# Kernel optimization log

Hardware: AMD Instinct MI355X
Metric: run time of the kernel (lower is better)

## Reference

```python
import jax, jax.numpy as jnp
import numpy as np

L, D_IN, D_HID, D_OUT, N = 8, 256, 1024, 256, 32768


def setup_inputs() -> dict:
    key = jax.random.key(0)
    kx, kp, kw1, kw2 = jax.random.split(key, 4)
    x = jax.random.normal(kx, (N, D_IN), dtype=jnp.float32)
    plane_idx = jax.random.randint(kp, (N,), 0, L, dtype=jnp.int32)
    W1 = jax.random.normal(kw1, (L, D_HID, D_IN), dtype=jnp.float32) * 0.014
    b1 = jnp.zeros((L, D_HID), dtype=jnp.float32)
    W2 = jax.random.normal(kw2, (L, D_OUT, D_HID), dtype=jnp.float32) * np.float32((2.0 / D_HID) ** 0.5)
    b2 = jnp.zeros((L, D_OUT), dtype=jnp.float32)
    return {"x": x, "W1": W1, "b1": b1, "W2": W2, "b2": b2, "plane_idx": plane_idx}


def reference(x, W1, b1, W2, b2, plane_idx):
    # Dense-dispatch MoE reference: scan over the L planes, run the full
    # 2-layer MLP for each plane's weights, and select per-walker rows via
    # the plane mask (equivalent math to gather -> MLP -> scatter).
    n_planes = W1.shape[0]
    out0 = jnp.zeros((x.shape[0], W2.shape[1]), dtype=x.dtype)

    def plane_step(out, p):
        h = jax.nn.gelu(x @ W1[p].T + b1[p], approximate=False)  # [N, D_hid]
        o = h @ W2[p].T + b2[p]                                  # [N, D_out]
        out = jnp.where((plane_idx == p)[:, None], o, out)
        return out, None

    out, _ = jax.lax.scan(plane_step, out0, jnp.arange(n_planes))
    return out
```

## Files before the change

kernel.cpp:

```cpp
#include <hip/hip_runtime.h>
#include <hip/hip_fp16.h>
#include <cstdint>

#define NT      32768
#define DIN     256
#define DHID    1024
#define DOUT    256
#define NPLANES 8
#define NBLK    (NT / 256)

typedef unsigned short u16;
typedef __attribute__((ext_vector_type(8))) _Float16 f16x8;
typedef __attribute__((ext_vector_type(4))) float    f32x4;

#define WS_OFFSETS 0
#define WS_META    64
#define WS_TP      1024
#define WS_TM      (WS_TP + 544*4)
#define WS_BLKHIST (WS_TM + 544*4)
#define WS_BLKBASE (WS_BLKHIST + NBLK*8*4)
#define WS_PERM    (WS_BLKBASE + NBLK*8*4)
#define WS_XB      (WS_PERM + NT*4)
#define WS_W1B     (WS_XB + NT*DIN*2)
#define WS_W2B     (WS_W1B + NPLANES*DHID*DIN*2)
#define WS_HB      (WS_W2B + NPLANES*DOUT*DHID*2)

__device__ __forceinline__ u16 f2h_bits(float f) {
    __half h = __float2half(f);
    return *reinterpret_cast<u16*>(&h);
}

__device__ __forceinline__ void gl_lds16(const void* g, void* l) {
    __builtin_amdgcn_global_load_lds(
        (const __attribute__((address_space(1))) void*)g,
        (__attribute__((address_space(3))) void*)l,
        16, 0, 0);
}

__global__ void prep_k(const int* __restrict__ pidx, const float* __restrict__ x,
                       const float* __restrict__ W1, const float* __restrict__ W2,
                       int* __restrict__ blkhist, u16* __restrict__ xb,
                       u16* __restrict__ w1b, u16* __restrict__ w2b) {
    __shared__ int cnt[NPLANES];
    const int t = threadIdx.x, lane = t & 63;
    if ((int)blockIdx.x < NBLK) {
        if (t < NPLANES) cnt[t] = 0;
        __syncthreads();
        const int p = pidx[blockIdx.x * 256 + t];
#pragma unroll
        for (int q = 0; q < NPLANES; ++q) {
            unsigned long long m = __ballot(p == q);
            if (p == q && __popcll(m & ((1ULL << lane) - 1)) == 0)
                atomicAdd(&cnt[q], __popcll(m));
        }
        __syncthreads();
        if (t < NPLANES) blkhist[blockIdx.x * NPLANES + t] = cnt[t];
    }
    const int n0 = NT * DIN / 4, n1 = NPLANES * DHID * DIN / 4, n2 = NPLANES * DOUT * DHID / 4;
    const int stride = gridDim.x * blockDim.x;
    for (int i = blockIdx.x * blockDim.x + t; i < n0 + n1 + n2; i += stride) {
        const float4* s; ushort4* d; int j;
        if (i < n0)           { s = (const float4*)x;  d = (ushort4*)xb;  j = i; }
        else if (i < n0 + n1) { s = (const float4*)W1; d = (ushort4*)w1b; j = i - n0; }
        else                  { s = (const float4*)W2; d = (ushort4*)w2b; j = i - n0 - n1; }
        float4 v = s[j];
        ushort4 o;
        o.x = f2h_bits(v.x); o.y = f2h_bits(v.y);
        o.z = f2h_bits(v.z); o.w = f2h_bits(v.w);
        d[j] = o;
    }
}

__global__ void scan_k(const int* __restrict__ blkhist, int* __restrict__ offsets,
                       int* __restrict__ blkbase, int* __restrict__ meta,
                       int* __restrict__ tp, int* __restrict__ tm) {
    __shared__ int tot[NPLANES];
    const int t = threadIdx.x;
    if (t < NPLANES) {
        int s = 0;
#pragma unroll 8
        for (int b = 0; b < NBLK; ++b) s += blkhist[b * NPLANES + t];
        tot[t] = s;
    }
    __syncthreads();
    if (t == 0) {
        int off = 0, tc = 0;
        for (int p = 0; p < NPLANES; ++p) {
            offsets[p] = off;
            for (int m = 0; m < tot[p]; m += 64) { tp[tc] = p; tm[tc] = m; ++tc; }
            off += tot[p];
        }
        offsets[NPLANES] = off;
        meta[0] = tc;
    }
    __syncthreads();
    if (t < NPLANES) {
        int run = offsets[t];
#pragma unroll 8
        for (int b = 0; b < NBLK; ++b) {
            blkbase[b * NPLANES + t] = run;
            run += blkhist[b * NPLANES + t];
        }
    }
}

__global__ void scatter_k(const int* __restrict__ pidx, const int* __restrict__ blkbase,
                          int* __restrict__ perm) {
    __shared__ int wcnt[4][NPLANES];
    __shared__ int wbase[4][NPLANES];
    const int t = threadIdx.x, lane = t & 63, wave = t >> 6;
    const int i = blockIdx.x * 256 + t;
    const int p = pidx[i];
    int rank = 0;
#pragma unroll
    for (int q = 0; q < NPLANES; ++q) {
        unsigned long long m = __ballot(p == q);
        if (lane == 0) wcnt[wave][q] = __popcll(m);
        if (p == q) rank = __popcll(m & ((1ULL << lane) - 1));
    }
    __syncthreads();
    if (t < NPLANES) {
        int run = blkbase[blockIdx.x * NPLANES + t];
#pragma unroll
        for (int w = 0; w < 4; ++w) { wbase[w][t] = run; run += wcnt[w][t]; }
    }
    __syncthreads();
    perm[wbase[wave][p] + rank] = i;
}

#define XCD_MAP(NSPLIT)                                                        \
    const int ntiles = meta[0];                                                \
    const int xcd = blockIdx.x & 7, idx = blockIdx.x >> 3;                     \
    const int q8 = ntiles >> 3, r8 = ntiles & 7;                               \
    const int tn = q8 + (xcd < r8 ? 1 : 0);                                    \
    if (idx >= tn * (NSPLIT)) return;                                          \
    const int tile = (xcd < r8 ? xcd * (q8 + 1)                                \
                               : r8 * (q8 + 1) + (xcd - r8) * q8)              \
                     + idx / (NSPLIT);                                         \
    const int n0v = (idx % (NSPLIT)) * 128;

__global__ __launch_bounds__(256, 4) void gemm1_k(
    const u16* __restrict__ xb, const u16* __restrict__ w1b,
    const float* __restrict__ b1, const int* __restrict__ perm,
    const int* __restrict__ offsets, const int* __restrict__ meta,
    const int* __restrict__ tp, const int* __restrict__ tm,
    u16* __restrict__ hb)
{
    __shared__ __align__(16) u16 smem[12288];
    XCD_MAP(8)
    const int p   = tp[tile];
    const int m0  = tm[tile];
    const int off = offsets[p];
    const int cnt = offsets[p + 1] - off;

    u16* const sA = smem;
    u16* const sB = smem + 4096;

    const int tid = threadIdx.x;
    const u16* aptr[2];
    const u16* bptr[4];
#pragma unroll
    for (int c = 0; c < 2; ++c) {
        const int slot = c * 256 + tid, row = slot >> 3, ch = slot & 7;
        const int gr = min(m0 + row, cnt - 1);
        aptr[c] = xb + (size_t)perm[off + gr] * DIN + ((ch ^ (row & 7)) * 8);
    }
#pragma unroll
    for (int c = 0; c < 4; ++c) {
        const int slot = c * 256 + tid, row = slot >> 3, ch = slot & 7;
        bptr[c] = w1b + ((size_t)p * DHID + n0v + row) * DIN + ((ch ^ (row & 7)) * 8);
    }
    const int wave = tid >> 6, lane = tid & 63;
    const int wr = wave >> 1, wc = wave & 1;
    const int lm = lane & 15, lk = lane >> 4;

    f32x4 acc[2][4];
#pragma unroll
    for (int a = 0; a < 2; ++a)
#pragma unroll
        for (int b = 0; b < 4; ++b) acc[a][b] = (f32x4){0.f, 0.f, 0.f, 0.f};

    for (int kt = 0; kt < DIN / 64; ++kt) {
        const int k0 = kt * 64;
#pragma unroll
        for (int c = 0; c < 2; ++c) gl_lds16(aptr[c] + k0, sA + c * 2048 + tid * 8);
#pragma unroll
        for (int c = 0; c < 4; ++c) gl_lds16(bptr[c] + k0, sB + c * 2048 + tid * 8);
        __syncthreads();
#pragma unroll
        for (int kk = 0; kk < 2; ++kk) {
            f16x8 af[2], bf[4];
#pragma unroll
            for (int mf = 0; mf < 2; ++mf) {
                const int row = wr * 32 + mf * 16 + lm;
                const int g   = kk * 4 + lk;
                af[mf] = *(const f16x8*)(sA + row * 64 + ((g ^ (row & 7)) * 8));
            }
#pragma unroll
            for (int nf = 0; nf < 4; ++nf) {
                const int row = wc * 64 + nf * 16 + lm;
                const int g   = kk * 4 + lk;
                bf[nf] = *(const f16x8*)(sB + row * 64 + ((g ^ (row & 7)) * 8));
            }
#pragma unroll
            for (int mf = 0; mf < 2; ++mf)
#pragma unroll
                for (int nf = 0; nf < 4; ++nf)
                    acc[mf][nf] = __builtin_amdgcn_mfma_f32_16x16x32_f16(
                        af[mf], bf[nf], acc[mf][nf], 0, 0, 0);
        }
        __syncthreads();
    }

    u16* const sOut = smem;
#pragma unroll
    for (int nf = 0; nf < 4; ++nf) {
        const int col = wc * 64 + nf * 16 + lm;
        const float bb = b1[p * DHID + n0v + col];
        const int cc = col >> 3, c7 = col & 7;
#pragma unroll
        for (int mf = 0; mf < 2; ++mf) {
#pragma unroll
            for (int j = 0; j < 4; ++j) {
                const int tok = wr * 32 + mf * 16 + lk * 4 + j;
                float v = acc[mf][nf][j] + bb;
                float g = 0.5f * v * (1.0f + erff(v * 0.70710678118654752f));
                sOut[tok * 128 + ((cc ^ (tok & 15)) * 8) + c7] = f2h_bits(g);
            }
        }
    }
    __syncthreads();
    const int r = tid >> 2, qq = tid & 3;
    if (m0 + r < cnt) {
        u16* dst = hb + (size_t)(off + m0 + r) * DHID + n0v;
#pragma unroll
        for (int c = 0; c < 4; ++c) {
            const int l = qq * 4 + c;
            *(int4*)(dst + l * 8) = *(const int4*)(sOut + r * 128 + ((l ^ (r & 15)) * 8));
        }
    }
}

__global__ __launch_bounds__(256, 4) void gemm2_k(
    const u16* __restrict__ hb, const u16* __restrict__ w2b,
    const float* __restrict__ b2, const int* __restrict__ perm,
    const int* __restrict__ offsets, const int* __restrict__ meta,
    const int* __restrict__ tp, const int* __restrict__ tm,
    float* __restrict__ out)
{
    __shared__ __align__(16) u16 smem[12288];
    XCD_MAP(2)
    const int p   = tp[tile];
    const int m0  = tm[tile];
    const int off = offsets[p];
    const int cnt = offsets[p + 1] - off;

    u16* const sA = smem;
    u16* const sB = smem + 4096;

    const int tid = threadIdx.x;
    const u16* aptr[2];
    const u16* bptr[4];
#pragma unroll
    for (int c = 0; c < 2; ++c) {
        const int slot = c * 256 + tid, row = slot >> 3, ch = slot & 7;
        aptr[c] = hb + (size_t)(off + min(m0 + row, cnt - 1)) * DHID + ((ch ^ (row & 7)) * 8);
    }
#pragma unroll
    for (int c = 0; c < 4; ++c) {
        const int slot = c * 256 + tid, row = slot >> 3, ch = slot & 7;
        bptr[c] = w2b + ((size_t)p * DOUT + n0v + row) * DHID + ((ch ^ (row & 7)) * 8);
    }
    const int wave = tid >> 6, lane = tid & 63;
    const int wr = wave >> 1, wc = wave & 1;
    const int lm = lane & 15, lk = lane >> 4;

    f32x4 acc[2][4];
#pragma unroll
    for (int a = 0; a < 2; ++a)
#pragma unroll
        for (int b = 0; b < 4; ++b) acc[a][b] = (f32x4){0.f, 0.f, 0.f, 0.f};

    for (int kt = 0; kt < DHID / 64; ++kt) {
        const int k0 = kt * 64;
#pragma unroll
        for (int c = 0; c < 2; ++c) gl_lds16(aptr[c] + k0, sA + c * 2048 + tid * 8);
#pragma unroll
        for (int c = 0; c < 4; ++c) gl_lds16(bptr[c] + k0, sB + c * 2048 + tid * 8);
        __syncthreads();
#pragma unroll
        for (int kk = 0; kk < 2; ++kk) {
            f16x8 af[2], bf[4];
#pragma unroll
            for (int mf = 0; mf < 2; ++mf) {
                const int row = wr * 32 + mf * 16 + lm;
                const int g   = kk * 4 + lk;
                af[mf] = *(const f16x8*)(sA + row * 64 + ((g ^ (row & 7)) * 8));
            }
#pragma unroll
            for (int nf = 0; nf < 4; ++nf) {
                const int row = wc * 64 + nf * 16 + lm;
                const int g   = kk * 4 + lk;
                bf[nf] = *(const f16x8*)(sB + row * 64 + ((g ^ (row & 7)) * 8));
            }
#pragma unroll
            for (int mf = 0; mf < 2; ++mf)
#pragma unroll
                for (int nf = 0; nf < 4; ++nf)
                    acc[mf][nf] = __builtin_amdgcn_mfma_f32_16x16x32_f16(
                        af[mf], bf[nf], acc[mf][nf], 0, 0, 0);
        }
        __syncthreads();
    }

#pragma unroll
    for (int nf = 0; nf < 4; ++nf) {
        const int col = n0v + wc * 64 + nf * 16 + lm;
        const float bb = b2[p * DOUT + col];
#pragma unroll
        for (int mf = 0; mf < 2; ++mf) {
#pragma unroll
            for (int j = 0; j < 4; ++j) {
                const int tok = wr * 32 + mf * 16 + lk * 4 + j;
                if (m0 + tok < cnt)
                    out[(size_t)perm[off + m0 + tok] * DOUT + col] = acc[mf][nf][j] + bb;
            }
        }
    }
}

extern "C" void kernel_launch(void* const* d_in, const int* in_sizes, int n_in,
                              void* d_out, int out_size, void* d_ws, size_t ws_size,
                              hipStream_t stream) {
    const float* x    = (const float*)d_in[0];
    const float* W1   = (const float*)d_in[1];
    const float* b1   = (const float*)d_in[2];
    const float* W2   = (const float*)d_in[3];
    const float* b2   = (const float*)d_in[4];
    const int*   pidx = (const int*)d_in[5];
    float*       out  = (float*)d_out;

    char* ws      = (char*)d_ws;
    int* offsets  = (int*)(ws + WS_OFFSETS);
    int* meta     = (int*)(ws + WS_META);
    int* tp       = (int*)(ws + WS_TP);
    int* tm       = (int*)(ws + WS_TM);
    int* blkhist  = (int*)(ws + WS_BLKHIST);
    int* blkbase  = (int*)(ws + WS_BLKBASE);
    int* perm     = (int*)(ws + WS_PERM);
    u16* xb       = (u16*)(ws + WS_XB);
    u16* w1b      = (u16*)(ws + WS_W1B);
    u16* w2b      = (u16*)(ws + WS_W2B);
    u16* hb       = (u16*)(ws + WS_HB);

    prep_k<<<2048, 256, 0, stream>>>(pidx, x, W1, W2, blkhist, xb, w1b, w2b);
    scan_k<<<1, 64, 0, stream>>>(blkhist, offsets, blkbase, meta, tp, tm);
    scatter_k<<<NBLK, 256, 0, stream>>>(pidx, blkbase, perm);

    gemm1_k<<<4224, 256, 0, stream>>>(xb, w1b, b1, perm, offsets, meta, tp, tm, hb);
    gemm2_k<<<1056, 256, 0, stream>>>(hb, w2b, b2, perm, offsets, meta, tp, tm, out);
}
```

Measured before the change: 115.5 us.

## Double-buffer gemm2 LDS loads, use sigmoid GELU approximation, retune launch bounds

The second GEMM now stages tiles into two LDS buffers, issuing global-to-LDS loads for the next K step before computing the current one. Partial vmcnt waits with raw barriers replace the full __syncthreads, so load latency can overlap MFMA work. The exact erf GELU in gemm1's epilogue is replaced by a tanh-form approximation built from exp and a hardware reciprocal, which cuts epilogue cost but changes numerics slightly. Launch bounds change to 6 waves/SIMD occupancy hints for gemm1 and 3 for gemm2, since the doubled LDS footprint lowers gemm2 occupancy.

```diff
diff --git a/kernel.cpp b/kernel.cpp
--- a/kernel.cpp
+++ b/kernel.cpp
@@ -35,6 +35,12 @@
         (const __attribute__((address_space(1))) void*)g,
         (__attribute__((address_space(3))) void*)l,
         16, 0, 0);
+}
+
+__device__ __forceinline__ float gelu_fast(float x) {
+    const float u = x * (1.5957691216f + 0.07135481283f * x * x);
+    const float e = __expf(-u);
+    return x * __builtin_amdgcn_rcpf(1.0f + e);
 }
 
 __global__ void prep_k(const int* __restrict__ pidx, const float* __restrict__ x,
@@ -139,7 +145,7 @@
                      + idx / (NSPLIT);                                         \
     const int n0v = (idx % (NSPLIT)) * 128;
 
-__global__ __launch_bounds__(256, 4) void gemm1_k(
+__global__ __launch_bounds__(256, 6) void gemm1_k(
     const u16* __restrict__ xb, const u16* __restrict__ w1b,
     const float* __restrict__ b1, const int* __restrict__ perm,
     const int* __restrict__ offsets, const int* __restrict__ meta,
@@ -223,9 +229,8 @@
 #pragma unroll
             for (int j = 0; j < 4; ++j) {
                 const int tok = wr * 32 + mf * 16 + lk * 4 + j;
-                float v = acc[mf][nf][j] + bb;
-                float g = 0.5f * v * (1.0f + erff(v * 0.70710678118654752f));
-                sOut[tok * 128 + ((cc ^ (tok & 15)) * 8) + c7] = f2h_bits(g);
+                sOut[tok * 128 + ((cc ^ (tok & 15)) * 8) + c7] =
+                    f2h_bits(gelu_fast(acc[mf][nf][j] + bb));
             }
         }
     }
@@ -241,23 +246,20 @@
     }
 }
 
-__global__ __launch_bounds__(256, 4) void gemm2_k(
+__global__ __launch_bounds__(256, 3) void gemm2_k(
     const u16* __restrict__ hb, const u16* __restrict__ w2b,
     const float* __restrict__ b2, const int* __restrict__ perm,
     const int* __restrict__ offsets, const int* __restrict__ meta,
     const int* __restrict__ tp, const int* __restrict__ tm,
     float* __restrict__ out)
 {
-    __shared__ __align__(16) u16 smem[12288];
+    __shared__ __align__(16) u16 smem[2][12288];
     XCD_MAP(2)
     const int p   = tp[tile];
     const int m0  = tm[tile];
     const int off = offsets[p];
     const int cnt = offsets[p + 1] - off;
 
-    u16* const sA = smem;
-    u16* const sB = smem + 4096;
-
     const int tid = threadIdx.x;
     const u16* aptr[2];
     const u16* bptr[4];
@@ -281,13 +283,31 @@
 #pragma unroll
         for (int b = 0; b < 4; ++b) acc[a][b] = (f32x4){0.f, 0.f, 0.f, 0.f};
 
-    for (int kt = 0; kt < DHID / 64; ++kt) {
-        const int k0 = kt * 64;
-#pragma unroll
-        for (int c = 0; c < 2; ++c) gl_lds16(aptr[c] + k0, sA + c * 2048 + tid * 8);
-#pragma unroll
-        for (int c = 0; c < 4; ++c) gl_lds16(bptr[c] + k0, sB + c * 2048 + tid * 8);
-        __syncthreads();
+#define STAGE2(dst, k0)                                                        \
+    do {                                                                       \
+        gl_lds16(aptr[0] + (k0), (dst) + tid * 8);                             \
+        gl_lds16(aptr[1] + (k0), (dst) + 2048 + tid * 8);                      \
+        gl_lds16(bptr[0] + (k0), (dst) + 4096 + tid * 8);                      \
+        gl_lds16(bptr[1] + (k0), (dst) + 6144 + tid * 8);                      \
+        gl_lds16(bptr[2] + (k0), (dst) + 8192 + tid * 8);                      \
+        gl_lds16(bptr[3] + (k0), (dst) + 10240 + tid * 8);                     \
+    } while (0)
+
+    STAGE2(&smem[0][0], 0);
+    asm volatile("s_waitcnt vmcnt(0)" ::: "memory");
+    __builtin_amdgcn_s_barrier();
+
+    constexpr int KT = DHID / 64;
+    for (int kt = 0; kt < KT; ++kt) {
+        const int cur = kt & 1;
+        u16* const bufc = &smem[cur][0];
+        if (kt + 1 < KT) {
+            STAGE2(&smem[cur ^ 1][0], (kt + 1) * 64);
+            asm volatile("s_waitcnt vmcnt(6)" ::: "memory");
+        } else {
+            asm volatile("s_waitcnt vmcnt(0)" ::: "memory");
+        }
+        __builtin_amdgcn_s_barrier();
 #pragma unroll
         for (int kk = 0; kk < 2; ++kk) {
             f16x8 af[2], bf[4];
@@ -295,13 +315,13 @@
             for (int mf = 0; mf < 2; ++mf) {
                 const int row = wr * 32 + mf * 16 + lm;
                 const int g   = kk * 4 + lk;
-                af[mf] = *(const f16x8*)(sA + row * 64 + ((g ^ (row & 7)) * 8));
+                af[mf] = *(const f16x8*)(bufc + row * 64 + ((g ^ (row & 7)) * 8));
             }
 #pragma unroll
             for (int nf = 0; nf < 4; ++nf) {
                 const int row = wc * 64 + nf * 16 + lm;
                 const int g   = kk * 4 + lk;
-                bf[nf] = *(const f16x8*)(sB + row * 64 + ((g ^ (row & 7)) * 8));
+                bf[nf] = *(const f16x8*)(bufc + 4096 + row * 64 + ((g ^ (row & 7)) * 8));
             }
 #pragma unroll
             for (int mf = 0; mf < 2; ++mf)
@@ -310,8 +330,9 @@
                     acc[mf][nf] = __builtin_amdgcn_mfma_f32_16x16x32_f16(
                         af[mf], bf[nf], acc[mf][nf], 0, 0, 0);
         }
-        __syncthreads();
-    }
+        __builtin_amdgcn_s_barrier();
+    }
+#undef STAGE2
 
 #pragma unroll
     for (int nf = 0; nf < 4; ++nf) {
```

New measurement: 115.1 us. No clear change (-0.4%).
